# Kernel tuning notes

Measured on AMD Instinct MI355X. Metric: run time of the kernel, lower is better.

Reference implementation:

```python
import jax, jax.numpy as jnp
import numpy as np

WS = 7  # window size
NH = 8  # num heads


def _relative_position_index(ws):
    coords = np.stack(np.meshgrid(np.arange(ws), np.arange(ws), indexing='ij'), axis=0)
    flat = coords.reshape(2, -1)                       # [2, ws*ws]
    rel = flat[:, :, None] - flat[:, None, :]          # [2, N, N]
    rel = rel.transpose(1, 2, 0)                       # [N, N, 2]
    xx = (rel[:, :, 0] + ws - 1) * (2 * ws - 1)
    yy = rel[:, :, 1] + ws - 1
    return jnp.asarray(xx + yy, dtype=jnp.int32)       # [N, N]


def setup_inputs() -> dict:
    key = jax.random.key(0)
    ks = jax.random.split(key, 6)
    B_, N, C = 4096, WS * WS, 256
    return {
        'x': jax.random.normal(ks[0], (B_, N, C), dtype=jnp.float32),
        'qkv_w': jax.random.normal(ks[1], (C, 3 * C), dtype=jnp.float32) * 0.02,
        'qkv_b': jax.random.normal(ks[2], (3 * C,), dtype=jnp.float32) * 0.02,
        'rpb_table': jax.random.normal(ks[3], ((2 * WS - 1) ** 2, NH), dtype=jnp.float32) * 0.02,
        'proj_w': jax.random.normal(ks[4], (C, C), dtype=jnp.float32) * 0.02,
        'proj_b': jax.random.normal(ks[5], (C,), dtype=jnp.float32) * 0.02,
    }


def reference(x, qkv_w, qkv_b, rpb_table, proj_w, proj_b):
    B_, N, C = x.shape
    D = C // NH
    scale = D ** -0.5
    rpi = _relative_position_index(WS)                  # [N, N] int

    qkv = x @ qkv_w + qkv_b                             # [B, N, 3C]
    qkv = qkv.reshape(B_, N, 3, NH, D).transpose(2, 0, 3, 1, 4)
    q, k, v = qkv[0], qkv[1], qkv[2]                    # each [B, H, N, D]

    attn = jnp.einsum('bhnd,bhmd->bhnm', q * scale, k)  # [B, H, N, N]
    bias = rpb_table[rpi.reshape(-1)].reshape(N, N, NH).transpose(2, 0, 1)
    attn = jax.nn.softmax(attn + bias[None], axis=-1)

    out = jnp.einsum('bhnm,bhmd->bhnd', attn, v)        # [B, H, N, D]
    out = out.transpose(0, 2, 1, 3).reshape(B_, N, C)
    return out @ proj_w + proj_b
```

## Files before the change

kernel.cpp:

```cpp
#include <hip/hip_runtime.h>
#include <stdint.h>


typedef __attribute__((ext_vector_type(8))) short bf16x8;
typedef __attribute__((ext_vector_type(4))) float f32x4;

#define PARTSZ 51380224
#define BHSTRIDE 1568
#define BSTRIDE 12544

__device__ __forceinline__ unsigned short f2bf(float f) {
    unsigned u = __float_as_uint(f);
    u += 0x7fffu + ((u >> 16) & 1u);
    return (unsigned short)(u >> 16);
}
__device__ __forceinline__ unsigned pk2(float a, float b) {
    return (unsigned)f2bf(a) | ((unsigned)f2bf(b) << 16);
}
__device__ __forceinline__ void gl2lds16(const void* gptr, void* lptr) {
    __builtin_amdgcn_global_load_lds(
        (const __attribute__((address_space(1))) unsigned int*)gptr,
        (__attribute__((address_space(3))) unsigned int*)lptr, 16, 0, 0);
}

__global__ void k_prep(const float* __restrict__ qkv_w, const float* __restrict__ proj_w,
                       short* __restrict__ Wqkv_t, short* __restrict__ Wproj_t) {
    int tid = blockIdx.x * 256 + threadIdx.x;
    if (tid < 196608) {
        int nn = tid >> 8, kk = tid & 255;
        Wqkv_t[tid] = (short)f2bf(qkv_w[kk * 768 + nn]);
    } else {
        int t2 = tid - 196608;
        int nn = t2 >> 8, kk = t2 & 255;
        Wproj_t[t2] = (short)f2bf(proj_w[kk * 256 + nn]);
    }
}

__global__ __launch_bounds__(256) void k_gemm_qkv(const float* __restrict__ x,
        const short* __restrict__ Wt, const float* __restrict__ bias,
        short* __restrict__ qkv) {
    __shared__ __align__(16) short As[128 * 32];
    __shared__ __align__(16) short Bs[128 * 32];
    int bx = blockIdx.x;
    int fblk = bx % 6, tblk = bx / 6;
    int F0 = fblk * 128, T0 = tblk * 128;
    int t = threadIdx.x;
    int wid = t >> 6, lane = t & 63;
    int l15 = lane & 15, g = lane >> 4;
    int wr = wid >> 1, wc = wid & 1;

    f32x4 acc[4][4];
    for (int i = 0; i < 4; i++)
        for (int j = 0; j < 4; j++) acc[i][j] = (f32x4){0.f, 0.f, 0.f, 0.f};

    int arow = t >> 1, acb = (t & 1) * 16;
    const float* asrc = x + (size_t)(T0 + arow) * 256 + acb;
    short* adst = &As[arow * 32 + acb];

    for (int ks = 0; ks < 8; ks++) {
        int k0 = ks * 32;
        const float4* s4 = (const float4*)(asrc + k0);
        float4 f0 = s4[0], f1 = s4[1], f2 = s4[2], f3 = s4[3];
        ((uint4*)adst)[0] = make_uint4(pk2(f0.x, f0.y), pk2(f0.z, f0.w),
                                       pk2(f1.x, f1.y), pk2(f1.z, f1.w));
        ((uint4*)adst)[1] = make_uint4(pk2(f2.x, f2.y), pk2(f2.z, f2.w),
                                       pk2(f3.x, f3.y), pk2(f3.z, f3.w));
        for (int i = 0; i < 2; i++) {
            int cbase = i * 256 + wid * 64;
            int c = cbase + lane;
            int brow = c >> 2, bseg = c & 3;
            gl2lds16(Wt + (size_t)(F0 + brow) * 256 + k0 + bseg * 8, &Bs[cbase * 8]);
        }
        __syncthreads();
        bf16x8 af[4], bfg[4];
        for (int it = 0; it < 4; it++)
            af[it] = *(const bf16x8*)&Bs[(wr * 64 + it * 16 + l15) * 32 + g * 8];
        for (int jt = 0; jt < 4; jt++)
            bfg[jt] = *(const bf16x8*)&As[(wc * 64 + jt * 16 + l15) * 32 + g * 8];
        for (int it = 0; it < 4; it++)
            for (int jt = 0; jt < 4; jt++)
                acc[it][jt] = __builtin_amdgcn_mfma_f32_16x16x32_bf16(
                    af[it], bfg[jt], acc[it][jt], 0, 0, 0);
        __syncthreads();
    }
    size_t tokoff[4];
    for (int jt = 0; jt < 4; jt++) {
        int m = T0 + wc * 64 + jt * 16 + l15;
        int b = m / 49, n = m - b * 49;
        tokoff[jt] = (size_t)b * BSTRIDE + (size_t)n * 32;
    }
    for (int it = 0; it < 4; it++) {
        int jr = F0 + wr * 64 + it * 16 + g * 4;
        int part = jr >> 8, hh = (jr >> 5) & 7, db = jr & 31;
        size_t ro = (size_t)part * PARTSZ + (size_t)hh * BHSTRIDE + db;
        float4 bv = *(const float4*)&bias[jr];
        for (int jt = 0; jt < 4; jt++) {
            unsigned* dst = (unsigned*)(qkv + ro + tokoff[jt]);
            dst[0] = pk2(acc[it][jt][0] + bv.x, acc[it][jt][1] + bv.y);
            dst[1] = pk2(acc[it][jt][2] + bv.z, acc[it][jt][3] + bv.w);
        }
    }
}

__global__ __launch_bounds__(256) void k_attn(const short* __restrict__ qkv,
        const float* __restrict__ rpb, short* __restrict__ aout) {
    __shared__ __align__(16) short smem[6912];
    __shared__ float rb[169];
    short* Qs = smem;
    short* Ks = smem + 2048;
    short* Pl = smem;
    short* Vt = smem + 4608;

    int bh = blockIdx.x;
    int h = bh & 7;
    int t = threadIdx.x;
    int w = t >> 6;
    int L = t & 63, l15 = L & 15, g = L >> 4;
    size_t base = (size_t)bh * BHSTRIDE;

    const char* Qg = (const char*)(qkv + base);
    const char* Kg = (const char*)(qkv + (size_t)PARTSZ + base);
    gl2lds16(Qg + w * 1024 + L * 16, Qs + w * 512);
    gl2lds16(Kg + w * 1024 + L * 16, Ks + w * 512);
    {
        int r = t >> 2, c = t & 3;
        const uint4* Vg4 = (const uint4*)(qkv + (size_t)2 * PARTSZ + base);
        uint4 v = Vg4[r * 4 + c];
        if (r >= 49) v = make_uint4(0u, 0u, 0u, 0u);
        unsigned vv[4] = {v.x, v.y, v.z, v.w};
        int d0 = c * 8;
        for (int i = 0; i < 4; i++) {
            Vt[(d0 + 2 * i) * 72 + r]     = (short)(vv[i] & 0xffffu);
            Vt[(d0 + 2 * i + 1) * 72 + r] = (short)(vv[i] >> 16);
        }
    }
    if (t < 169) rb[t] = rpb[t * 8 + h];
    __syncthreads();

    bf16x8 ka[4], qb;
    for (int mt = 0; mt < 4; mt++)
        ka[mt] = *(const bf16x8*)&Ks[(mt * 16 + l15) * 32 + g * 8];
    qb = *(const bf16x8*)&Qs[(w * 16 + l15) * 32 + g * 8];
    f32x4 zero = {0.f, 0.f, 0.f, 0.f};
    f32x4 s[4];
    for (int mt = 0; mt < 4; mt++)
        s[mt] = __builtin_amdgcn_mfma_f32_16x16x32_bf16(ka[mt], qb, zero, 0, 0, 0);
    __syncthreads();

    const float scale = 0.17677669529663687f;
    int n = w * 16 + l15;
    int ni = n / 7;
    int an = 13 * ni + (n - 7 * ni) + 84;
    for (int mt = 0; mt < 4; mt++)
        for (int r = 0; r < 4; r++) {
            int m = mt * 16 + g * 4 + r;
            int mi = m / 7;
            int idx = an - (13 * mi + (m - 7 * mi));
            idx = idx < 0 ? 0 : (idx > 168 ? 168 : idx);
            float val = s[mt][r] * scale + rb[idx];
            s[mt][r] = (m < 49) ? val : -1e30f;
        }
    float tmax = -1e30f;
    for (int mt = 0; mt < 4; mt++)
        for (int r = 0; r < 4; r++) tmax = fmaxf(tmax, s[mt][r]);
    tmax = fmaxf(tmax, __shfl_xor(tmax, 16));
    tmax = fmaxf(tmax, __shfl_xor(tmax, 32));
    float rsum = 0.f;
    for (int mt = 0; mt < 4; mt++)
        for (int r = 0; r < 4; r++) {
            float e = __expf(s[mt][r] - tmax);
            s[mt][r] = e;
            rsum += e;
        }
    rsum += __shfl_xor(rsum, 16);
    rsum += __shfl_xor(rsum, 32);

    for (int mt = 0; mt < 4; mt++) {
        unsigned* dst = (unsigned*)&Pl[(w * 16 + l15) * 72 + mt * 16 + g * 4];
        dst[0] = pk2(s[mt][0], s[mt][1]);
        dst[1] = pk2(s[mt][2], s[mt][3]);
    }
    __syncthreads();

    bf16x8 va[2][2], pb[2];
    for (int dt = 0; dt < 2; dt++)
        for (int kk = 0; kk < 2; kk++)
            va[dt][kk] = *(const bf16x8*)&Vt[(dt * 16 + l15) * 72 + kk * 32 + g * 8];
    for (int kk = 0; kk < 2; kk++)
        pb[kk] = *(const bf16x8*)&Pl[(w * 16 + l15) * 72 + kk * 32 + g * 8];
    f32x4 o[2];
    for (int dt = 0; dt < 2; dt++) {
        f32x4 a = zero;
        for (int kk = 0; kk < 2; kk++)
            a = __builtin_amdgcn_mfma_f32_16x16x32_bf16(va[dt][kk], pb[kk], a, 0, 0, 0);
        o[dt] = a;
    }
    if (n < 49) {
        float inv = 1.f / rsum;
        size_t ob = (size_t)((bh >> 3) * 49 + n) * 256 + h * 32;
        for (int dt = 0; dt < 2; dt++) {
            unsigned* dst = (unsigned*)(aout + ob + dt * 16 + g * 4);
            dst[0] = pk2(o[dt][0] * inv, o[dt][1] * inv);
            dst[1] = pk2(o[dt][2] * inv, o[dt][3] * inv);
        }
    }
}

__global__ __launch_bounds__(256) void k_gemm_proj(const short* __restrict__ A,
        const short* __restrict__ Wt, const float* __restrict__ bias,
        float* __restrict__ out) {
    __shared__ __align__(16) short As[128 * 32];
    __shared__ __align__(16) short Bs[128 * 32];
    int bx = blockIdx.x;
    int fblk = bx & 1, tblk = bx >> 1;
    int F0 = fblk * 128, T0 = tblk * 128;
    int t = threadIdx.x;
    int wid = t >> 6, lane = t & 63;
    int l15 = lane & 15, g = lane >> 4;
    int wr = wid >> 1, wc = wid & 1;

    f32x4 acc[4][4];
    for (int i = 0; i < 4; i++)
        for (int j = 0; j < 4; j++) acc[i][j] = (f32x4){0.f, 0.f, 0.f, 0.f};

    for (int ks = 0; ks < 8; ks++) {
        int k0 = ks * 32;
        for (int i = 0; i < 2; i++) {
            int cbase = i * 256 + wid * 64;
            int c = cbase + lane;
            int row = c >> 2, seg = c & 3;
            gl2lds16(A + (size_t)(T0 + row) * 256 + k0 + seg * 8, &As[cbase * 8]);
            gl2lds16(Wt + (size_t)(F0 + row) * 256 + k0 + seg * 8, &Bs[cbase * 8]);
        }
        __syncthreads();
        bf16x8 af[4], bfg[4];
        for (int it = 0; it < 4; it++)
            af[it] = *(const bf16x8*)&Bs[(wr * 64 + it * 16 + l15) * 32 + g * 8];
        for (int jt = 0; jt < 4; jt++)
            bfg[jt] = *(const bf16x8*)&As[(wc * 64 + jt * 16 + l15) * 32 + g * 8];
        for (int it = 0; it < 4; it++)
            for (int jt = 0; jt < 4; jt++)
                acc[it][jt] = __builtin_amdgcn_mfma_f32_16x16x32_bf16(
                    af[it], bfg[jt], acc[it][jt], 0, 0, 0);
        __syncthreads();
    }
    int mtok[4];
    for (int jt = 0; jt < 4; jt++) mtok[jt] = T0 + wc * 64 + jt * 16 + l15;
    for (int it = 0; it < 4; it++) {
        int jr = F0 + wr * 64 + it * 16 + g * 4;
        float4 bv = *(const float4*)&bias[jr];
        for (int jt = 0; jt < 4; jt++) {
            float4 val = make_float4(acc[it][jt][0] + bv.x, acc[it][jt][1] + bv.y,
                                     acc[it][jt][2] + bv.z, acc[it][jt][3] + bv.w);
            *(float4*)&out[(size_t)mtok[jt] * 256 + jr] = val;
        }
    }
}

extern "C" void kernel_launch(void* const* d_in, const int* in_sizes, int n_in,
                              void* d_out, int out_size, void* d_ws, size_t ws_size,
                              hipStream_t stream) {
    const float* x      = (const float*)d_in[0];
    const float* qkv_w  = (const float*)d_in[1];
    const float* qkv_b  = (const float*)d_in[2];
    const float* rpb    = (const float*)d_in[3];
    const float* proj_w = (const float*)d_in[4];
    const float* proj_b = (const float*)d_in[5];
    float* out = (float*)d_out;

    short* Wqkv_t  = (short*)d_ws;
    short* Wproj_t = Wqkv_t + 768 * 256;
    short* qkv     = Wproj_t + 256 * 256;
    short* aout    = qkv + (size_t)3 * PARTSZ;
    if (ws_size < 411566080ull) return;

    k_prep<<<1024, 256, 0, stream>>>(qkv_w, proj_w, Wqkv_t, Wproj_t);
    k_gemm_qkv<<<9408, 256, 0, stream>>>(x, Wqkv_t, qkv_b, qkv);
    k_attn<<<32768, 256, 0, stream>>>(qkv, rpb, aout);
    k_gemm_proj<<<3136, 256, 0, stream>>>(aout, Wproj_t, proj_b, out);
}
```

Baseline: 703.0 us.

## Pre-convert x to bf16, XOR-swizzle LDS tiles, and remap GEMM block order

Moves the fp32-to-bf16 conversion of x into the prep kernel, writing a bf16 copy into the aout buffer so the QKV GEMM can stage A with direct global-to-LDS loads instead of per-tile conversion. Both GEMMs now XOR-swizzle the 16-byte segments in LDS so MFMA fragment reads hit fewer bank conflicts. Block indices are remapped in groups of 8 to change which tiles run together, likely for cache locality. The cost is an extra full pass over x (read fp32, write bf16), which takes memory traffic in exchange for cheaper GEMM staging, and aout is reused as scratch for xb.

```diff
diff --git a/kernel.cpp b/kernel.cpp
--- a/kernel.cpp
+++ b/kernel.cpp
@@ -23,60 +23,65 @@
         (__attribute__((address_space(3))) unsigned int*)lptr, 16, 0, 0);
 }
 
-__global__ void k_prep(const float* __restrict__ qkv_w, const float* __restrict__ proj_w,
+__global__ void k_prep(const float* __restrict__ x,
+                       const float* __restrict__ qkv_w, const float* __restrict__ proj_w,
+                       short* __restrict__ xb,
                        short* __restrict__ Wqkv_t, short* __restrict__ Wproj_t) {
-    int tid = blockIdx.x * 256 + threadIdx.x;
-    if (tid < 196608) {
-        int nn = tid >> 8, kk = tid & 255;
-        Wqkv_t[tid] = (short)f2bf(qkv_w[kk * 768 + nn]);
+    int b = blockIdx.x;
+    if (b < 25088) {
+        size_t i = ((size_t)b * 256 + threadIdx.x) * 8;
+        const float4* s = (const float4*)(x + i);
+        float4 f0 = s[0], f1 = s[1];
+        *(uint4*)(xb + i) = make_uint4(pk2(f0.x, f0.y), pk2(f0.z, f0.w),
+                                       pk2(f1.x, f1.y), pk2(f1.z, f1.w));
     } else {
-        int t2 = tid - 196608;
-        int nn = t2 >> 8, kk = t2 & 255;
-        Wproj_t[t2] = (short)f2bf(proj_w[kk * 256 + nn]);
-    }
-}
-
-__global__ __launch_bounds__(256) void k_gemm_qkv(const float* __restrict__ x,
+        int tid = (b - 25088) * 256 + threadIdx.x;
+        if (tid < 196608) {
+            int nn = tid >> 8, kk = tid & 255;
+            Wqkv_t[tid] = (short)f2bf(qkv_w[kk * 768 + nn]);
+        } else {
+            int t2 = tid - 196608;
+            int nn = t2 >> 8, kk = t2 & 255;
+            Wproj_t[t2] = (short)f2bf(proj_w[kk * 256 + nn]);
+        }
+    }
+}
+
+__global__ __launch_bounds__(256) void k_gemm_qkv(const short* __restrict__ xb,
         const short* __restrict__ Wt, const float* __restrict__ bias,
         short* __restrict__ qkv) {
     __shared__ __align__(16) short As[128 * 32];
     __shared__ __align__(16) short Bs[128 * 32];
-    int bx = blockIdx.x;
-    int fblk = bx % 6, tblk = bx / 6;
+    int b = blockIdx.x;
+    int lb = (b & 7) * 1176 + (b >> 3);
+    int fblk = lb % 6, tblk = lb / 6;
     int F0 = fblk * 128, T0 = tblk * 128;
     int t = threadIdx.x;
     int wid = t >> 6, lane = t & 63;
     int l15 = lane & 15, g = lane >> 4;
     int wr = wid >> 1, wc = wid & 1;
+    int cs = (g ^ ((l15 >> 1) & 3)) * 8;
 
     f32x4 acc[4][4];
     for (int i = 0; i < 4; i++)
         for (int j = 0; j < 4; j++) acc[i][j] = (f32x4){0.f, 0.f, 0.f, 0.f};
 
-    int arow = t >> 1, acb = (t & 1) * 16;
-    const float* asrc = x + (size_t)(T0 + arow) * 256 + acb;
-    short* adst = &As[arow * 32 + acb];
-
     for (int ks = 0; ks < 8; ks++) {
         int k0 = ks * 32;
-        const float4* s4 = (const float4*)(asrc + k0);
-        float4 f0 = s4[0], f1 = s4[1], f2 = s4[2], f3 = s4[3];
-        ((uint4*)adst)[0] = make_uint4(pk2(f0.x, f0.y), pk2(f0.z, f0.w),
-                                       pk2(f1.x, f1.y), pk2(f1.z, f1.w));
-        ((uint4*)adst)[1] = make_uint4(pk2(f2.x, f2.y), pk2(f2.z, f2.w),
-                                       pk2(f3.x, f3.y), pk2(f3.z, f3.w));
         for (int i = 0; i < 2; i++) {
             int cbase = i * 256 + wid * 64;
             int c = cbase + lane;
-            int brow = c >> 2, bseg = c & 3;
-            gl2lds16(Wt + (size_t)(F0 + brow) * 256 + k0 + bseg * 8, &Bs[cbase * 8]);
+            int row = c >> 2;
+            int seg = (c & 3) ^ ((c >> 3) & 3);
+            gl2lds16(xb + (size_t)(T0 + row) * 256 + k0 + seg * 8, &As[cbase * 8]);
+            gl2lds16(Wt + (size_t)(F0 + row) * 256 + k0 + seg * 8, &Bs[cbase * 8]);
         }
         __syncthreads();
         bf16x8 af[4], bfg[4];
         for (int it = 0; it < 4; it++)
-            af[it] = *(const bf16x8*)&Bs[(wr * 64 + it * 16 + l15) * 32 + g * 8];
+            af[it] = *(const bf16x8*)&Bs[(wr * 64 + it * 16 + l15) * 32 + cs];
         for (int jt = 0; jt < 4; jt++)
-            bfg[jt] = *(const bf16x8*)&As[(wc * 64 + jt * 16 + l15) * 32 + g * 8];
+            bfg[jt] = *(const bf16x8*)&As[(wc * 64 + jt * 16 + l15) * 32 + cs];
         for (int it = 0; it < 4; it++)
             for (int jt = 0; jt < 4; jt++)
                 acc[it][jt] = __builtin_amdgcn_mfma_f32_16x16x32_bf16(
@@ -86,8 +91,8 @@
     size_t tokoff[4];
     for (int jt = 0; jt < 4; jt++) {
         int m = T0 + wc * 64 + jt * 16 + l15;
-        int b = m / 49, n = m - b * 49;
-        tokoff[jt] = (size_t)b * BSTRIDE + (size_t)n * 32;
+        int bb = m / 49, n = m - bb * 49;
+        tokoff[jt] = (size_t)bb * BSTRIDE + (size_t)n * 32;
     }
     for (int it = 0; it < 4; it++) {
         int jr = F0 + wr * 64 + it * 16 + g * 4;
@@ -211,13 +216,15 @@
         float* __restrict__ out) {
     __shared__ __align__(16) short As[128 * 32];
     __shared__ __align__(16) short Bs[128 * 32];
-    int bx = blockIdx.x;
-    int fblk = bx & 1, tblk = bx >> 1;
+    int b = blockIdx.x;
+    int lb = (b & 7) * 392 + (b >> 3);
+    int fblk = lb & 1, tblk = lb >> 1;
     int F0 = fblk * 128, T0 = tblk * 128;
     int t = threadIdx.x;
     int wid = t >> 6, lane = t & 63;
     int l15 = lane & 15, g = lane >> 4;
     int wr = wid >> 1, wc = wid & 1;
+    int cs = (g ^ ((l15 >> 1) & 3)) * 8;
 
     f32x4 acc[4][4];
     for (int i = 0; i < 4; i++)
@@ -228,16 +235,17 @@
         for (int i = 0; i < 2; i++) {
             int cbase = i * 256 + wid * 64;
             int c = cbase + lane;
-            int row = c >> 2, seg = c & 3;
+            int row = c >> 2;
+            int seg = (c & 3) ^ ((c >> 3) & 3);
             gl2lds16(A + (size_t)(T0 + row) * 256 + k0 + seg * 8, &As[cbase * 8]);
             gl2lds16(Wt + (size_t)(F0 + row) * 256 + k0 + seg * 8, &Bs[cbase * 8]);
         }
         __syncthreads();
         bf16x8 af[4], bfg[4];
         for (int it = 0; it < 4; it++)
-            af[it] = *(const bf16x8*)&Bs[(wr * 64 + it * 16 + l15) * 32 + g * 8];
+            af[it] = *(const bf16x8*)&Bs[(wr * 64 + it * 16 + l15) * 32 + cs];
         for (int jt = 0; jt < 4; jt++)
-            bfg[jt] = *(const bf16x8*)&As[(wc * 64 + jt * 16 + l15) * 32 + g * 8];
+            bfg[jt] = *(const bf16x8*)&As[(wc * 64 + jt * 16 + l15) * 32 + cs];
         for (int it = 0; it < 4; it++)
             for (int jt = 0; jt < 4; jt++)
                 acc[it][jt] = __builtin_amdgcn_mfma_f32_16x16x32_bf16(
@@ -272,10 +280,11 @@
     short* Wproj_t = Wqkv_t + 768 * 256;
     short* qkv     = Wproj_t + 256 * 256;
     short* aout    = qkv + (size_t)3 * PARTSZ;
+    short* xb      = aout;
     if (ws_size < 411566080ull) return;
 
-    k_prep<<<1024, 256, 0, stream>>>(qkv_w, proj_w, Wqkv_t, Wproj_t);
-    k_gemm_qkv<<<9408, 256, 0, stream>>>(x, Wqkv_t, qkv_b, qkv);
+    k_prep<<<26112, 256, 0, stream>>>(x, qkv_w, proj_w, xb, Wqkv_t, Wproj_t);
+    k_gemm_qkv<<<9408, 256, 0, stream>>>(xb, Wqkv_t, qkv_b, qkv);
     k_attn<<<32768, 256, 0, stream>>>(qkv, rpb, aout);
     k_gemm_proj<<<3136, 256, 0, stream>>>(aout, Wproj_t, proj_b, out);
 }
```

Result: no change. 697.2 us (-0.8%).

## Fuse QKV GEMM, window attention and projection into one per-window kernel

Applied to the files above, without the earlier changes.

Replaces the three-kernel pipeline (QKV GEMM, attention, projection) with a single kernel where each 512-thread block handles one 49-token window. Q, K, V^T and the attention output stay in LDS, so the large bf16 qkv and attention-output tensors never go to global memory. The kernel streams weight tiles into LDS with double buffering and XOR-swizzled layouts. In exchange each block recomputes from streamed weights with small 64-token tiles, uses heavy LDS (~150KB, one block per CU) and many barriers, and pads 15 of 64 token rows with wasted MFMA work.

```diff
diff --git a/kernel.cpp b/kernel.cpp
--- a/kernel.cpp
+++ b/kernel.cpp
@@ -4,10 +4,6 @@
 
 typedef __attribute__((ext_vector_type(8))) short bf16x8;
 typedef __attribute__((ext_vector_type(4))) float f32x4;
-
-#define PARTSZ 51380224
-#define BHSTRIDE 1568
-#define BSTRIDE 12544
 
 __device__ __forceinline__ unsigned short f2bf(float f) {
     unsigned u = __float_as_uint(f);
@@ -36,223 +32,217 @@
     }
 }
 
-__global__ __launch_bounds__(256) void k_gemm_qkv(const float* __restrict__ x,
-        const short* __restrict__ Wt, const float* __restrict__ bias,
-        short* __restrict__ qkv) {
-    __shared__ __align__(16) short As[128 * 32];
-    __shared__ __align__(16) short Bs[128 * 32];
-    int bx = blockIdx.x;
-    int fblk = bx % 6, tblk = bx / 6;
-    int F0 = fblk * 128, T0 = tblk * 128;
-    int t = threadIdx.x;
-    int wid = t >> 6, lane = t & 63;
-    int l15 = lane & 15, g = lane >> 4;
-    int wr = wid >> 1, wc = wid & 1;
-
-    f32x4 acc[4][4];
-    for (int i = 0; i < 4; i++)
-        for (int j = 0; j < 4; j++) acc[i][j] = (f32x4){0.f, 0.f, 0.f, 0.f};
-
-    int arow = t >> 1, acb = (t & 1) * 16;
-    const float* asrc = x + (size_t)(T0 + arow) * 256 + acb;
-    short* adst = &As[arow * 32 + acb];
-
-    for (int ks = 0; ks < 8; ks++) {
-        int k0 = ks * 32;
-        const float4* s4 = (const float4*)(asrc + k0);
-        float4 f0 = s4[0], f1 = s4[1], f2 = s4[2], f3 = s4[3];
-        ((uint4*)adst)[0] = make_uint4(pk2(f0.x, f0.y), pk2(f0.z, f0.w),
-                                       pk2(f1.x, f1.y), pk2(f1.z, f1.w));
-        ((uint4*)adst)[1] = make_uint4(pk2(f2.x, f2.y), pk2(f2.z, f2.w),
-                                       pk2(f3.x, f3.y), pk2(f3.z, f3.w));
-        for (int i = 0; i < 2; i++) {
-            int cbase = i * 256 + wid * 64;
-            int c = cbase + lane;
-            int brow = c >> 2, bseg = c & 3;
-            gl2lds16(Wt + (size_t)(F0 + brow) * 256 + k0 + bseg * 8, &Bs[cbase * 8]);
-        }
-        __syncthreads();
-        bf16x8 af[4], bfg[4];
-        for (int it = 0; it < 4; it++)
-            af[it] = *(const bf16x8*)&Bs[(wr * 64 + it * 16 + l15) * 32 + g * 8];
-        for (int jt = 0; jt < 4; jt++)
-            bfg[jt] = *(const bf16x8*)&As[(wc * 64 + jt * 16 + l15) * 32 + g * 8];
-        for (int it = 0; it < 4; it++)
-            for (int jt = 0; jt < 4; jt++)
-                acc[it][jt] = __builtin_amdgcn_mfma_f32_16x16x32_bf16(
-                    af[it], bfg[jt], acc[it][jt], 0, 0, 0);
-        __syncthreads();
-    }
-    size_t tokoff[4];
-    for (int jt = 0; jt < 4; jt++) {
-        int m = T0 + wc * 64 + jt * 16 + l15;
-        int b = m / 49, n = m - b * 49;
-        tokoff[jt] = (size_t)b * BSTRIDE + (size_t)n * 32;
-    }
-    for (int it = 0; it < 4; it++) {
-        int jr = F0 + wr * 64 + it * 16 + g * 4;
-        int part = jr >> 8, hh = (jr >> 5) & 7, db = jr & 31;
-        size_t ro = (size_t)part * PARTSZ + (size_t)hh * BHSTRIDE + db;
-        float4 bv = *(const float4*)&bias[jr];
-        for (int jt = 0; jt < 4; jt++) {
-            unsigned* dst = (unsigned*)(qkv + ro + tokoff[jt]);
-            dst[0] = pk2(acc[it][jt][0] + bv.x, acc[it][jt][1] + bv.y);
-            dst[1] = pk2(acc[it][jt][2] + bv.z, acc[it][jt][3] + bv.w);
-        }
-    }
-}
-
-__global__ __launch_bounds__(256) void k_attn(const short* __restrict__ qkv,
-        const float* __restrict__ rpb, short* __restrict__ aout) {
-    __shared__ __align__(16) short smem[6912];
-    __shared__ float rb[169];
-    short* Qs = smem;
-    short* Ks = smem + 2048;
-    short* Pl = smem;
-    short* Vt = smem + 4608;
-
-    int bh = blockIdx.x;
-    int h = bh & 7;
-    int t = threadIdx.x;
-    int w = t >> 6;
-    int L = t & 63, l15 = L & 15, g = L >> 4;
-    size_t base = (size_t)bh * BHSTRIDE;
-
-    const char* Qg = (const char*)(qkv + base);
-    const char* Kg = (const char*)(qkv + (size_t)PARTSZ + base);
-    gl2lds16(Qg + w * 1024 + L * 16, Qs + w * 512);
-    gl2lds16(Kg + w * 1024 + L * 16, Ks + w * 512);
+#define QS_OFF 0
+#define KS_OFF 16384
+#define VT_OFF 32768
+#define XS_OFF 51200
+#define PL_OFF 51200
+#define WS_OFF 67584
+
+__global__ __launch_bounds__(512, 1) void k_fused(
+        const float* __restrict__ x, const short* __restrict__ Wq,
+        const short* __restrict__ Wp, const float* __restrict__ qkv_b,
+        const float* __restrict__ rpb, const float* __restrict__ proj_b,
+        float* __restrict__ out) {
+    __shared__ __align__(16) short smem[75776];
+    __shared__ float rpbs[1352];
+
+    const int b = blockIdx.x;
+    const int t = threadIdx.x;
+    const int w = t >> 6, lane = t & 63;
+    const int l15 = lane & 15, g = lane >> 4;
+    const int wr = w >> 1, wc = w & 1;
+    const int cs8 = (l15 >> 1) & 3;
+    const int swz = (g ^ cs8) << 3;
+
+    const int srow = t >> 2;
+    const int sseg = (t & 3) ^ ((t >> 3) & 3);
+
+    f32x4 zero = {0.f, 0.f, 0.f, 0.f};
+
+    gl2lds16(Wq + (size_t)srow * 256 + sseg * 8, &smem[WS_OFF + t * 8]);
+    for (int i = t; i < 1352; i += 512) rpbs[i] = rpb[i];
+    for (int i = 0; i < 4; i++) {
+        int cid = t + i * 512;
+        int tok = cid >> 5, c = cid & 31;
+        uint4 w4 = make_uint4(0u, 0u, 0u, 0u);
+        if (tok < 49) {
+            const float4* s = (const float4*)(x + ((size_t)b * 49 + tok) * 256 + c * 8);
+            float4 f0 = s[0], f1 = s[1];
+            w4 = make_uint4(pk2(f0.x, f0.y), pk2(f0.z, f0.w),
+                            pk2(f1.x, f1.y), pk2(f1.z, f1.w));
+        }
+        *(uint4*)&smem[XS_OFF + tok * 256 + ((c ^ (tok & 7)) << 3)] = w4;
+    }
+    __syncthreads();
+
+    int buf = 0;
+    for (int fblk = 0; fblk < 6; fblk++) {
+        f32x4 acc[2][2];
+        for (int i = 0; i < 2; i++)
+            for (int j = 0; j < 2; j++) acc[i][j] = zero;
+        for (int ks = 0; ks < 8; ks++) {
+            int st = fblk * 8 + ks;
+            if (st < 47) {
+                int nf = (st + 1) >> 3, nk = (st + 1) & 7;
+                gl2lds16(Wq + (size_t)(nf * 128 + srow) * 256 + nk * 32 + sseg * 8,
+                         &smem[WS_OFF + (buf ^ 1) * 4096 + t * 8]);
+            }
+            const short* Wb = &smem[WS_OFF + buf * 4096];
+            bf16x8 af0 = *(const bf16x8*)&Wb[(wr * 32 + l15) * 32 + swz];
+            bf16x8 af1 = *(const bf16x8*)&Wb[(wr * 32 + 16 + l15) * 32 + swz];
+            int tok0 = wc * 32 + l15;
+            int xsl = (((ks << 2) + g) ^ (l15 & 7)) << 3;
+            bf16x8 bf0 = *(const bf16x8*)&smem[XS_OFF + tok0 * 256 + xsl];
+            bf16x8 bf1 = *(const bf16x8*)&smem[XS_OFF + (tok0 + 16) * 256 + xsl];
+            acc[0][0] = __builtin_amdgcn_mfma_f32_16x16x32_bf16(af0, bf0, acc[0][0], 0, 0, 0);
+            acc[0][1] = __builtin_amdgcn_mfma_f32_16x16x32_bf16(af0, bf1, acc[0][1], 0, 0, 0);
+            acc[1][0] = __builtin_amdgcn_mfma_f32_16x16x32_bf16(af1, bf0, acc[1][0], 0, 0, 0);
+            acc[1][1] = __builtin_amdgcn_mfma_f32_16x16x32_bf16(af1, bf1, acc[1][1], 0, 0, 0);
+            __syncthreads();
+            buf ^= 1;
+        }
+        for (int i2 = 0; i2 < 2; i2++) {
+            int f = fblk * 128 + wr * 32 + i2 * 16 + g * 4;
+            int part = f >> 8, h = (f >> 5) & 7, d0 = f & 31;
+            float4 bv = *(const float4*)&qkv_b[f];
+            for (int j2 = 0; j2 < 2; j2++) {
+                int tok = wc * 32 + j2 * 16 + l15;
+                float v0 = acc[i2][j2][0] + bv.x, v1 = acc[i2][j2][1] + bv.y;
+                float v2 = acc[i2][j2][2] + bv.z, v3 = acc[i2][j2][3] + bv.w;
+                if (part < 2) {
+                    int bo = (part ? KS_OFF : QS_OFF) + h * 2048 + tok * 32;
+                    unsigned* dst = (unsigned*)&smem[bo + (((d0 >> 3) ^ cs8) << 3) + (d0 & 7)];
+                    dst[0] = pk2(v0, v1);
+                    dst[1] = pk2(v2, v3);
+                } else {
+                    short* vt = &smem[VT_OFF + h * 2304 + tok];
+                    vt[(d0 + 0) * 72] = (short)f2bf(v0);
+                    vt[(d0 + 1) * 72] = (short)f2bf(v1);
+                    vt[(d0 + 2) * 72] = (short)f2bf(v2);
+                    vt[(d0 + 3) * 72] = (short)f2bf(v3);
+                }
+            }
+        }
+    }
+    __syncthreads();
+
     {
-        int r = t >> 2, c = t & 3;
-        const uint4* Vg4 = (const uint4*)(qkv + (size_t)2 * PARTSZ + base);
-        uint4 v = Vg4[r * 4 + c];
-        if (r >= 49) v = make_uint4(0u, 0u, 0u, 0u);
-        unsigned vv[4] = {v.x, v.y, v.z, v.w};
-        int d0 = c * 8;
-        for (int i = 0; i < 4; i++) {
-            Vt[(d0 + 2 * i) * 72 + r]     = (short)(vv[i] & 0xffffu);
-            Vt[(d0 + 2 * i + 1) * 72 + r] = (short)(vv[i] >> 16);
-        }
-    }
-    if (t < 169) rb[t] = rpb[t * 8 + h];
+        const int h = w;
+        const short* Kb = &smem[KS_OFF + h * 2048];
+        const short* Qb = &smem[QS_OFF + h * 2048];
+        bf16x8 ka[4], qb4[4], va[2][2];
+        for (int mt = 0; mt < 4; mt++)
+            ka[mt] = *(const bf16x8*)&Kb[(mt * 16 + l15) * 32 + swz];
+        for (int nt = 0; nt < 4; nt++)
+            qb4[nt] = *(const bf16x8*)&Qb[(nt * 16 + l15) * 32 + swz];
+        for (int dt = 0; dt < 2; dt++)
+            for (int kk = 0; kk < 2; kk++)
+                va[dt][kk] = *(const bf16x8*)&smem[VT_OFF + h * 2304 +
+                                                  (dt * 16 + l15) * 72 + kk * 32 + g * 8];
+        short* Plw = &smem[PL_OFF + w * 1152];
+        short* AOw = &smem[QS_OFF + h * 2048];
+        const float scale = 0.17677669529663687f;
+
+        for (int nt = 0; nt < 4; nt++) {
+            f32x4 s4[4];
+            for (int mt = 0; mt < 4; mt++)
+                s4[mt] = __builtin_amdgcn_mfma_f32_16x16x32_bf16(ka[mt], qb4[nt], zero, 0, 0, 0);
+            int n = nt * 16 + l15;
+            int ni = n / 7;
+            int an = 13 * ni + (n - 7 * ni) + 84;
+            for (int mt = 0; mt < 4; mt++)
+                for (int r = 0; r < 4; r++) {
+                    int m = mt * 16 + g * 4 + r;
+                    int mi = m / 7;
+                    int idx = an - (13 * mi + (m - 7 * mi));
+                    idx = idx < 0 ? 0 : (idx > 168 ? 168 : idx);
+                    float val = s4[mt][r] * scale + rpbs[idx * 8 + h];
+                    s4[mt][r] = (m < 49) ? val : -1e30f;
+                }
+            float tmax = -1e30f;
+            for (int mt = 0; mt < 4; mt++)
+                for (int r = 0; r < 4; r++) tmax = fmaxf(tmax, s4[mt][r]);
+            tmax = fmaxf(tmax, __shfl_xor(tmax, 16));
+            tmax = fmaxf(tmax, __shfl_xor(tmax, 32));
+            float rsum = 0.f;
+            for (int mt = 0; mt < 4; mt++)
+                for (int r = 0; r < 4; r++) {
+                    float e = __expf(s4[mt][r] - tmax);
+                    s4[mt][r] = e;
+                    rsum += e;
+                }
+            rsum += __shfl_xor(rsum, 16);
+            rsum += __shfl_xor(rsum, 32);
+
+            for (int mt = 0; mt < 4; mt++) {
+                unsigned* dst = (unsigned*)&Plw[l15 * 72 + mt * 16 + g * 4];
+                dst[0] = pk2(s4[mt][0], s4[mt][1]);
+                dst[1] = pk2(s4[mt][2], s4[mt][3]);
+            }
+            __syncthreads();
+
+            bf16x8 pb0 = *(const bf16x8*)&Plw[l15 * 72 + g * 8];
+            bf16x8 pb1 = *(const bf16x8*)&Plw[l15 * 72 + 32 + g * 8];
+            f32x4 o0 = __builtin_amdgcn_mfma_f32_16x16x32_bf16(va[0][0], pb0, zero, 0, 0, 0);
+            o0 = __builtin_amdgcn_mfma_f32_16x16x32_bf16(va[0][1], pb1, o0, 0, 0, 0);
+            f32x4 o1 = __builtin_amdgcn_mfma_f32_16x16x32_bf16(va[1][0], pb0, zero, 0, 0, 0);
+            o1 = __builtin_amdgcn_mfma_f32_16x16x32_bf16(va[1][1], pb1, o1, 0, 0, 0);
+            float inv = 1.f / rsum;
+            {
+                int d0 = g * 4;
+                unsigned* dst = (unsigned*)&AOw[n * 32 + (((d0 >> 3) ^ cs8) << 3) + (d0 & 7)];
+                dst[0] = pk2(o0[0] * inv, o0[1] * inv);
+                dst[1] = pk2(o0[2] * inv, o0[3] * inv);
+            }
+            {
+                int d0 = 16 + g * 4;
+                unsigned* dst = (unsigned*)&AOw[n * 32 + (((d0 >> 3) ^ cs8) << 3) + (d0 & 7)];
+                dst[0] = pk2(o1[0] * inv, o1[1] * inv);
+                dst[1] = pk2(o1[2] * inv, o1[3] * inv);
+            }
+            __syncthreads();
+        }
+    }
+
+    buf = 0;
+    gl2lds16(Wp + (size_t)srow * 256 + sseg * 8, &smem[WS_OFF + t * 8]);
     __syncthreads();
-
-    bf16x8 ka[4], qb;
-    for (int mt = 0; mt < 4; mt++)
-        ka[mt] = *(const bf16x8*)&Ks[(mt * 16 + l15) * 32 + g * 8];
-    qb = *(const bf16x8*)&Qs[(w * 16 + l15) * 32 + g * 8];
-    f32x4 zero = {0.f, 0.f, 0.f, 0.f};
-    f32x4 s[4];
-    for (int mt = 0; mt < 4; mt++)
-        s[mt] = __builtin_amdgcn_mfma_f32_16x16x32_bf16(ka[mt], qb, zero, 0, 0, 0);
-    __syncthreads();
-
-    const float scale = 0.17677669529663687f;
-    int n = w * 16 + l15;
-    int ni = n / 7;
-    int an = 13 * ni + (n - 7 * ni) + 84;
-    for (int mt = 0; mt < 4; mt++)
-        for (int r = 0; r < 4; r++) {
-            int m = mt * 16 + g * 4 + r;
-            int mi = m / 7;
-            int idx = an - (13 * mi + (m - 7 * mi));
-            idx = idx < 0 ? 0 : (idx > 168 ? 168 : idx);
-            float val = s[mt][r] * scale + rb[idx];
-            s[mt][r] = (m < 49) ? val : -1e30f;
-        }
-    float tmax = -1e30f;
-    for (int mt = 0; mt < 4; mt++)
-        for (int r = 0; r < 4; r++) tmax = fmaxf(tmax, s[mt][r]);
-    tmax = fmaxf(tmax, __shfl_xor(tmax, 16));
-    tmax = fmaxf(tmax, __shfl_xor(tmax, 32));
-    float rsum = 0.f;
-    for (int mt = 0; mt < 4; mt++)
-        for (int r = 0; r < 4; r++) {
-            float e = __expf(s[mt][r] - tmax);
-            s[mt][r] = e;
-            rsum += e;
-        }
-    rsum += __shfl_xor(rsum, 16);
-    rsum += __shfl_xor(rsum, 32);
-
-    for (int mt = 0; mt < 4; mt++) {
-        unsigned* dst = (unsigned*)&Pl[(w * 16 + l15) * 72 + mt * 16 + g * 4];
-        dst[0] = pk2(s[mt][0], s[mt][1]);
-        dst[1] = pk2(s[mt][2], s[mt][3]);
-    }
-    __syncthreads();
-
-    bf16x8 va[2][2], pb[2];
-    for (int dt = 0; dt < 2; dt++)
-        for (int kk = 0; kk < 2; kk++)
-            va[dt][kk] = *(const bf16x8*)&Vt[(dt * 16 + l15) * 72 + kk * 32 + g * 8];
-    for (int kk = 0; kk < 2; kk++)
-        pb[kk] = *(const bf16x8*)&Pl[(w * 16 + l15) * 72 + kk * 32 + g * 8];
-    f32x4 o[2];
-    for (int dt = 0; dt < 2; dt++) {
-        f32x4 a = zero;
-        for (int kk = 0; kk < 2; kk++)
-            a = __builtin_amdgcn_mfma_f32_16x16x32_bf16(va[dt][kk], pb[kk], a, 0, 0, 0);
-        o[dt] = a;
-    }
-    if (n < 49) {
-        float inv = 1.f / rsum;
-        size_t ob = (size_t)((bh >> 3) * 49 + n) * 256 + h * 32;
-        for (int dt = 0; dt < 2; dt++) {
-            unsigned* dst = (unsigned*)(aout + ob + dt * 16 + g * 4);
-            dst[0] = pk2(o[dt][0] * inv, o[dt][1] * inv);
-            dst[1] = pk2(o[dt][2] * inv, o[dt][3] * inv);
-        }
-    }
-}
-
-__global__ __launch_bounds__(256) void k_gemm_proj(const short* __restrict__ A,
-        const short* __restrict__ Wt, const float* __restrict__ bias,
-        float* __restrict__ out) {
-    __shared__ __align__(16) short As[128 * 32];
-    __shared__ __align__(16) short Bs[128 * 32];
-    int bx = blockIdx.x;
-    int fblk = bx & 1, tblk = bx >> 1;
-    int F0 = fblk * 128, T0 = tblk * 128;
-    int t = threadIdx.x;
-    int wid = t >> 6, lane = t & 63;
-    int l15 = lane & 15, g = lane >> 4;
-    int wr = wid >> 1, wc = wid & 1;
-
-    f32x4 acc[4][4];
-    for (int i = 0; i < 4; i++)
-        for (int j = 0; j < 4; j++) acc[i][j] = (f32x4){0.f, 0.f, 0.f, 0.f};
-
-    for (int ks = 0; ks < 8; ks++) {
-        int k0 = ks * 32;
-        for (int i = 0; i < 2; i++) {
-            int cbase = i * 256 + wid * 64;
-            int c = cbase + lane;
-            int row = c >> 2, seg = c & 3;
-            gl2lds16(A + (size_t)(T0 + row) * 256 + k0 + seg * 8, &As[cbase * 8]);
-            gl2lds16(Wt + (size_t)(F0 + row) * 256 + k0 + seg * 8, &Bs[cbase * 8]);
-        }
-        __syncthreads();
-        bf16x8 af[4], bfg[4];
-        for (int it = 0; it < 4; it++)
-            af[it] = *(const bf16x8*)&Bs[(wr * 64 + it * 16 + l15) * 32 + g * 8];
-        for (int jt = 0; jt < 4; jt++)
-            bfg[jt] = *(const bf16x8*)&As[(wc * 64 + jt * 16 + l15) * 32 + g * 8];
-        for (int it = 0; it < 4; it++)
-            for (int jt = 0; jt < 4; jt++)
-                acc[it][jt] = __builtin_amdgcn_mfma_f32_16x16x32_bf16(
-                    af[it], bfg[jt], acc[it][jt], 0, 0, 0);
-        __syncthreads();
-    }
-    int mtok[4];
-    for (int jt = 0; jt < 4; jt++) mtok[jt] = T0 + wc * 64 + jt * 16 + l15;
-    for (int it = 0; it < 4; it++) {
-        int jr = F0 + wr * 64 + it * 16 + g * 4;
-        float4 bv = *(const float4*)&bias[jr];
-        for (int jt = 0; jt < 4; jt++) {
-            float4 val = make_float4(acc[it][jt][0] + bv.x, acc[it][jt][1] + bv.y,
-                                     acc[it][jt][2] + bv.z, acc[it][jt][3] + bv.w);
-            *(float4*)&out[(size_t)mtok[jt] * 256 + jr] = val;
+    for (int foblk = 0; foblk < 2; foblk++) {
+        f32x4 acc[2][2];
+        for (int i = 0; i < 2; i++)
+            for (int j = 0; j < 2; j++) acc[i][j] = zero;
+        for (int ks = 0; ks < 8; ks++) {
+            int st = foblk * 8 + ks;
+            if (st < 15) {
+                int nf = (st + 1) >> 3, nk = (st + 1) & 7;
+                gl2lds16(Wp + (size_t)(nf * 128 + srow) * 256 + nk * 32 + sseg * 8,
+                         &smem[WS_OFF + (buf ^ 1) * 4096 + t * 8]);
+            }
+            const short* Wb = &smem[WS_OFF + buf * 4096];
+            bf16x8 af0 = *(const bf16x8*)&Wb[(wr * 32 + l15) * 32 + swz];
+            bf16x8 af1 = *(const bf16x8*)&Wb[(wr * 32 + 16 + l15) * 32 + swz];
+            int tok0 = wc * 32 + l15;
+            bf16x8 bf0 = *(const bf16x8*)&smem[QS_OFF + ks * 2048 + tok0 * 32 + swz];
+            bf16x8 bf1 = *(const bf16x8*)&smem[QS_OFF + ks * 2048 + (tok0 + 16) * 32 + swz];
+            acc[0][0] = __builtin_amdgcn_mfma_f32_16x16x32_bf16(af0, bf0, acc[0][0], 0, 0, 0);
+            acc[0][1] = __builtin_amdgcn_mfma_f32_16x16x32_bf16(af0, bf1, acc[0][1], 0, 0, 0);
+            acc[1][0] = __builtin_amdgcn_mfma_f32_16x16x32_bf16(af1, bf0, acc[1][0], 0, 0, 0);
+            acc[1][1] = __builtin_amdgcn_mfma_f32_16x16x32_bf16(af1, bf1, acc[1][1], 0, 0, 0);
+            __syncthreads();
+            buf ^= 1;
+        }
+        for (int i2 = 0; i2 < 2; i2++) {
+            int fo = foblk * 128 + wr * 32 + i2 * 16 + g * 4;
+            float4 bv = *(const float4*)&proj_b[fo];
+            for (int j2 = 0; j2 < 2; j2++) {
+                int tok = wc * 32 + j2 * 16 + l15;
+                if (tok < 49) {
+                    float4 val = make_float4(acc[i2][j2][0] + bv.x, acc[i2][j2][1] + bv.y,
+                                             acc[i2][j2][2] + bv.z, acc[i2][j2][3] + bv.w);
+                    *(float4*)&out[((size_t)b * 49 + tok) * 256 + fo] = val;
+                }
+            }
         }
     }
 }
@@ -270,12 +260,8 @@
 
     short* Wqkv_t  = (short*)d_ws;
     short* Wproj_t = Wqkv_t + 768 * 256;
-    short* qkv     = Wproj_t + 256 * 256;
-    short* aout    = qkv + (size_t)3 * PARTSZ;
-    if (ws_size < 411566080ull) return;
+    if (ws_size < 524288ull) return;
 
     k_prep<<<1024, 256, 0, stream>>>(qkv_w, proj_w, Wqkv_t, Wproj_t);
-    k_gemm_qkv<<<9408, 256, 0, stream>>>(x, Wqkv_t, qkv_b, qkv);
-    k_attn<<<32768, 256, 0, stream>>>(qkv, rpb, aout);
-    k_gemm_proj<<<3136, 256, 0, stream>>>(aout, Wproj_t, proj_b, out);
-}
+    k_fused<<<4096, 512, 0, stream>>>(x, Wqkv_t, Wproj_t, qkv_b, rpb, proj_b, out);
+}
```

Result: slower. 951.0 us (+35.3%).
